# Performance work log

Measured on AMD Instinct MI355X. Metric: run time of the kernel, lower is better.

The kernel has to match this reference:

```python
import jax, jax.numpy as jnp
import numpy as np

L = 4          # num_layers
D = 512        # gconv_dim == tlayer_dim
HG, CG = 8, 64 # gconv heads, head dim (D//8)
HT, CT = 4, 128  # tlayer heads, head dim
FF = 4 * D
G, NPG = 128, 256
N = G * NPG
E = N * 16
AF, AV = 9, 64   # atom features / vocab
BF, BV = 3, 8    # bond features / vocab
OUT = 128
SCALE = 0.02


def setup_inputs() -> dict:
    key = jax.random.key(0)
    ks = iter(jax.random.split(key, 64))
    rn = lambda shape: (jax.random.normal(next(ks), shape, dtype=jnp.float32) * SCALE)
    inp = {}
    # float params (stacked over layers)
    inp['atom_emb'] = rn((AF, AV, D))
    inp['bond_emb'] = rn((BF, BV, D))
    for nm in ['gq_w', 'gk_w', 'gv_w', 'ge_w', 'gskip_w', 'mid_w']:
        inp[nm] = rn((L, D, D))
    for nm in ['gq_b', 'gk_b', 'gv_b', 'gskip_b', 'mid_b']:
        inp[nm] = rn((L, D))
    inp['mid_g'] = jnp.ones((L, D), jnp.float32)
    inp['mid_bt'] = jnp.zeros((L, D), jnp.float32)
    for nm in ['tq_w', 'tk_w', 'tv_w', 'to_w']:
        inp[nm] = rn((L, D, D))
    for nm in ['tq_b', 'tk_b', 'tv_b', 'to_b']:
        inp[nm] = rn((L, D))
    inp['ln1_g'] = jnp.ones((L, D), jnp.float32)
    inp['ln1_b'] = jnp.zeros((L, D), jnp.float32)
    inp['f1_w'] = rn((L, D, FF))
    inp['f1_b'] = rn((L, FF))
    inp['f2_w'] = rn((L, FF, D))
    inp['f2_b'] = rn((L, D))
    inp['ln2_g'] = jnp.ones((L, D), jnp.float32)
    inp['ln2_b'] = jnp.zeros((L, D), jnp.float32)
    inp['out_w'] = rn((D, OUT))
    inp['out_b'] = rn((OUT,))
    # int inputs
    inp['x'] = jax.random.randint(next(ks), (N, AF), 0, AV, dtype=jnp.int32)
    inp['edge_attr'] = jax.random.randint(next(ks), (E, BF), 0, BV, dtype=jnp.int32)
    # intra-graph edges: random offsets within each graph
    gid = jax.random.randint(next(ks), (E,), 0, G, dtype=jnp.int32)
    src = gid * NPG + jax.random.randint(next(ks), (E,), 0, NPG, dtype=jnp.int32)
    dst = gid * NPG + jax.random.randint(next(ks), (E,), 0, NPG, dtype=jnp.int32)
    inp['edge_index'] = jnp.stack([src, dst])
    inp['batch'] = jnp.repeat(jnp.arange(G, dtype=jnp.int32), NPG)
    return inp


def _ln(x, g, b, eps=1e-5):
    mu = x.mean(-1, keepdims=True)
    var = ((x - mu) ** 2).mean(-1, keepdims=True)
    return (x - mu) * jax.lax.rsqrt(var + eps) * g + b


def _forward(atom_emb, bond_emb, gq_w, gq_b, gk_w, gk_b, gv_w, gv_b, ge_w,
             gskip_w, gskip_b, mid_w, mid_b, mid_g, mid_bt,
             tq_w, tq_b, tk_w, tk_b, tv_w, tv_b, to_w, to_b,
             ln1_g, ln1_b, f1_w, f1_b, f2_w, f2_b, ln2_g, ln2_b,
             out_w, out_b, x, edge_index, edge_attr, batch):
    # encoders: sum of per-feature embeddings (OGB AtomEncoder/BondEncoder)
    h = atom_emb[jnp.arange(AF)[None, :], x].sum(1)          # [N, D]
    e_attr = bond_emb[jnp.arange(BF)[None, :], edge_attr].sum(1)  # [E, D]
    src, dst = edge_index[0], edge_index[1]

    for i in range(L):
        # --- TransformerConv (PyG): edge-conditioned multi-head graph attention
        q = (h @ gq_w[i] + gq_b[i]).reshape(N, HG, CG)
        k = (h @ gk_w[i] + gk_b[i]).reshape(N, HG, CG)
        v = (h @ gv_w[i] + gv_b[i]).reshape(N, HG, CG)
        ee = (e_attr @ ge_w[i]).reshape(E, HG, CG)           # lin_edge (no bias)
        ke = k[src] + ee
        ve = v[src] + ee
        logits = (q[dst] * ke).sum(-1) / np.sqrt(CG)          # [E, HG]
        m = jax.ops.segment_max(logits, dst, num_segments=N)
        p = jnp.exp(logits - m[dst])
        denom = jax.ops.segment_sum(p, dst, num_segments=N) + 1e-16
        alpha = p / denom[dst]
        agg = jax.ops.segment_sum(alpha[..., None] * ve, dst, num_segments=N)
        h = agg.reshape(N, D) + h @ gskip_w[i] + gskip_b[i]   # root skip
        # --- middle Linear + LayerNorm + ReLU
        h = jax.nn.relu(_ln(h @ mid_w[i] + mid_b[i], mid_g[i], mid_bt[i]))

    xg = h.reshape(G, NPG, D)
    for i in range(L):
        # --- transformer encoder layer, dense attention within each graph
        q = (xg @ tq_w[i] + tq_b[i]).reshape(G, NPG, HT, CT)
        k = (xg @ tk_w[i] + tk_b[i]).reshape(G, NPG, HT, CT)
        v = (xg @ tv_w[i] + tv_b[i]).reshape(G, NPG, HT, CT)
        attn = jax.nn.softmax(jnp.einsum('gqhc,gkhc->ghqk', q, k) / np.sqrt(CT), axis=-1)
        o = jnp.einsum('ghqk,gkhc->gqhc', attn, v).reshape(G, NPG, D)
        xg = _ln(xg + (o @ to_w[i] + to_b[i]), ln1_g[i], ln1_b[i])
        ff = jax.nn.relu(xg @ f1_w[i] + f1_b[i]) @ f2_w[i] + f2_b[i]
        xg = _ln(xg + ff, ln2_g[i], ln2_b[i])

    # mean readout over nodes per graph (segment mean via batch)
    hflat = xg.reshape(N, D)
    cnt = jax.ops.segment_sum(jnp.ones((N,), hflat.dtype), batch, num_segments=G)
    pooled = jax.ops.segment_sum(hflat, batch, num_segments=G) / cnt[:, None]
    return pooled @ out_w + out_b                              # [G, OUT]


def reference(atom_emb, bond_emb, gq_w, gq_b, gk_w, gk_b, gv_w, gv_b, ge_w,
              gskip_w, gskip_b, mid_w, mid_b, mid_g, mid_bt,
              tq_w, tq_b, tk_w, tk_b, tv_w, tv_b, to_w, to_b,
              ln1_g, ln1_b, f1_w, f1_b, f2_w, f2_b, ln2_g, ln2_b,
              out_w, out_b, x, edge_index, edge_attr, batch):
    return _forward(atom_emb, bond_emb, gq_w, gq_b, gk_w, gk_b, gv_w, gv_b, ge_w,
                    gskip_w, gskip_b, mid_w, mid_b, mid_g, mid_bt,
                    tq_w, tq_b, tk_w, tk_b, tv_w, tv_b, to_w, to_b,
                    ln1_g, ln1_b, f1_w, f1_b, f2_w, f2_b, ln2_g, ln2_b,
                    out_w, out_b, x, edge_index, edge_attr, batch)
```

## Files before the change

### kernel.cpp

```cpp
#include <hip/hip_runtime.h>
#include <hip/hip_bf16.h>
#include <math.h>

#define N_NODES 32768
#define DIM     512
#define NE      524288
#define NL      4
#define NG      128
#define NPG_    256
#define HG_     8
#define CG_     64
#define HT_     4
#define CT_     128
#define FF_     2048
#define AF_     9
#define AV_     64
#define BV_     8
#define OUTD    128

typedef unsigned short u16;
typedef __attribute__((ext_vector_type(8))) short bhalf8;
typedef __attribute__((ext_vector_type(4))) float floatx4;
typedef __attribute__((ext_vector_type(8))) unsigned short u16x8;
typedef __attribute__((ext_vector_type(4))) unsigned short u16x4;

__device__ __forceinline__ u16 f2bf(float f) {
  union { float f; unsigned u; } x; x.f = f;
  unsigned r = x.u + 0x7fffu + ((x.u >> 16) & 1u);
  return (u16)(r >> 16);
}
__device__ __forceinline__ float bf2f(u16 u) {
  union { unsigned u; float f; } x; x.u = ((unsigned)u) << 16; return x.f;
}

#define GL2LDS(gp, lp) __builtin_amdgcn_global_load_lds( \
    (const __attribute__((address_space(1))) unsigned int*)(gp), \
    (__attribute__((address_space(3))) unsigned int*)(lp), 16, 0, 0)

__global__ __launch_bounds__(128) void atom_enc_kernel(
    const float* __restrict__ emb, const int* __restrict__ x, u16* __restrict__ hb) {
  int n = blockIdx.x;
  int d4 = threadIdx.x;
  const int* xr = x + n * AF_;
  float4 acc = {0.f, 0.f, 0.f, 0.f};
#pragma unroll
  for (int f = 0; f < AF_; ++f) {
    int idx = xr[f];
    const float4 v = *(const float4*)&emb[((size_t)(f * AV_ + idx)) * DIM + 4 * d4];
    acc.x += v.x; acc.y += v.y; acc.z += v.z; acc.w += v.w;
  }
  u16x4 o;
  o[0] = f2bf(acc.x); o[1] = f2bf(acc.y); o[2] = f2bf(acc.z); o[3] = f2bf(acc.w);
  *(u16x4*)&hb[(size_t)n * DIM + 4 * d4] = o;
}

__global__ __launch_bounds__(512) void bemb_proj_kernel(
    const float* __restrict__ bond_emb, const float* __restrict__ gew, u16* __restrict__ tab) {
  __shared__ float red[8][64];
  int r = blockIdx.x;
  int col = (threadIdx.x & 63) + blockIdx.y * 64;
  int kp = threadIdx.x >> 6;
  const float* a = bond_emb + (size_t)r * DIM + kp * 64;
  const float* w = gew + (size_t)kp * 64 * DIM + col;
  float acc = 0.f;
#pragma unroll 8
  for (int kx = 0; kx < 64; ++kx)
    acc += a[kx] * w[(size_t)kx * DIM];
  red[kp][threadIdx.x & 63] = acc;
  __syncthreads();
  if (threadIdx.x < 64) {
    float s = 0.f;
#pragma unroll
    for (int p = 0; p < 8; ++p) s += red[p][threadIdx.x];
    tab[(size_t)r * DIM + col] = f2bf(s);
  }
}

__global__ __launch_bounds__(256) void wcvt_kernel(
    const float* __restrict__ W, u16* __restrict__ Wt, int K, int N) {
  __shared__ float t[32][33];
  const size_t mo = (size_t)blockIdx.z * K * N;
  int k0 = blockIdx.y * 32, n0 = blockIdx.x * 32;
  int tx = threadIdx.x & 31, ty = threadIdx.x >> 5;
#pragma unroll
  for (int i = 0; i < 32; i += 8)
    t[ty + i][tx] = W[mo + (size_t)(k0 + ty + i) * N + n0 + tx];
  __syncthreads();
#pragma unroll
  for (int i = 0; i < 32; i += 8)
    Wt[mo + (size_t)(n0 + ty + i) * K + k0 + tx] = f2bf(t[tx][ty + i]);
}

__global__ __launch_bounds__(256) void gemm_mfma_kernel(
    const u16* __restrict__ A, const u16* __restrict__ Bt,
    const float* __restrict__ bias, float* __restrict__ Cf, u16* __restrict__ Cb,
    int K, int Nout, int relu, int bf16out, int vtout) {
  __shared__ __align__(16) u16 As[4096];
  __shared__ __align__(16) u16 Bs[4096];
  const int tid = threadIdx.x;
  const int wave = tid >> 6, lane = tid & 63;
  const int bm = blockIdx.y * 128, bn = blockIdx.x * 128;
  const int wr = wave >> 1, wc = wave & 1;

  const size_t rowA = (size_t)bm + (tid >> 2);
  const size_t rowB = (size_t)bn + (tid >> 2);
  const int gofs = (tid & 3) * 8;
  const u16* pA = A + rowA * K + gofs;
  const u16* pB = Bt + rowB * K + gofs;
  u16* lA0 = &As[wave * 512];
  u16* lB0 = &Bs[wave * 512];
  const size_t skip64 = (size_t)64 * K;

  floatx4 acc[4][4] = {};
  const int r = lane & 15, kg = lane >> 4;
  const int aoff = (wr * 64 + r) * 32 + kg * 8;
  const int boff = (wc * 64 + r) * 32 + kg * 8;

  for (int k0 = 0; k0 < K; k0 += 32) {
    GL2LDS(pA + k0, lA0);
    GL2LDS(pA + skip64 + k0, lA0 + 2048);
    GL2LDS(pB + k0, lB0);
    GL2LDS(pB + skip64 + k0, lB0 + 2048);
    __syncthreads();
    bhalf8 af[4], bg[4];
#pragma unroll
    for (int mi = 0; mi < 4; ++mi) af[mi] = *(const bhalf8*)&As[aoff + mi * 512];
#pragma unroll
    for (int ni = 0; ni < 4; ++ni) bg[ni] = *(const bhalf8*)&Bs[boff + ni * 512];
#pragma unroll
    for (int mi = 0; mi < 4; ++mi)
#pragma unroll
      for (int ni = 0; ni < 4; ++ni)
        acc[mi][ni] = __builtin_amdgcn_mfma_f32_16x16x32_bf16(af[mi], bg[ni], acc[mi][ni], 0, 0, 0);
    __syncthreads();
  }

  const int rb = (lane >> 4) * 4;
  const int cc = lane & 15;
#pragma unroll
  for (int mi = 0; mi < 4; ++mi) {
#pragma unroll
    for (int ni = 0; ni < 4; ++ni) {
      int gr0 = bm + wr * 64 + mi * 16 + rb;
      int gc = bn + wc * 64 + ni * 16 + cc;
      float bv = bias[gc];
#pragma unroll
      for (int reg = 0; reg < 4; ++reg) {
        int gr = gr0 + reg;
        float v = acc[mi][ni][reg] + bv;
        if (relu) v = fmaxf(v, 0.f);
        if (vtout)        Cb[((size_t)(gr >> 8) * DIM + gc) * NPG_ + (gr & 255)] = f2bf(v);
        else if (bf16out) Cb[(size_t)gr * Nout + gc] = f2bf(v);
        else              Cf[(size_t)gr * Nout + gc] = v;
      }
    }
  }
}

__global__ __launch_bounds__(256) void attn_s_mfma_kernel(
    const u16* __restrict__ q, const u16* __restrict__ k, u16* __restrict__ S, int zbase) {
  __shared__ __align__(16) u16 As[4096];
  __shared__ __align__(16) u16 Bs[4096];
  const int tid = threadIdx.x;
  const int wave = tid >> 6, lane = tid & 63;
  const int zl = blockIdx.z, z = zbase + zl, g = z >> 2, hh = z & 3;
  const int bm = blockIdx.y * 128, bn = blockIdx.x * 128;
  const int wr = wave >> 1, wc = wave & 1;
  const u16* qg = q + (size_t)g * NPG_ * DIM + hh * CT_;
  const u16* kg2 = k + (size_t)g * NPG_ * DIM + hh * CT_;
  const u16* pA = qg + (size_t)(bm + (tid >> 2)) * DIM + (tid & 3) * 8;
  const u16* pB = kg2 + (size_t)(bn + (tid >> 2)) * DIM + (tid & 3) * 8;
  u16* lA0 = &As[wave * 512];
  u16* lB0 = &Bs[wave * 512];
  const size_t skip64 = (size_t)64 * DIM;
  floatx4 acc[4][4] = {};
  const int r = lane & 15, kg_ = lane >> 4;
  const int aoff = (wr * 64 + r) * 32 + kg_ * 8;
  const int boff = (wc * 64 + r) * 32 + kg_ * 8;
  for (int k0 = 0; k0 < CT_; k0 += 32) {
    GL2LDS(pA + k0, lA0);
    GL2LDS(pA + skip64 + k0, lA0 + 2048);
    GL2LDS(pB + k0, lB0);
    GL2LDS(pB + skip64 + k0, lB0 + 2048);
    __syncthreads();
    bhalf8 af[4], bg[4];
#pragma unroll
    for (int mi = 0; mi < 4; ++mi) af[mi] = *(const bhalf8*)&As[aoff + mi * 512];
#pragma unroll
    for (int ni = 0; ni < 4; ++ni) bg[ni] = *(const bhalf8*)&Bs[boff + ni * 512];
#pragma unroll
    for (int mi = 0; mi < 4; ++mi)
#pragma unroll
      for (int ni = 0; ni < 4; ++ni)
        acc[mi][ni] = __builtin_amdgcn_mfma_f32_16x16x32_bf16(af[mi], bg[ni], acc[mi][ni], 0, 0, 0);
    __syncthreads();
  }
  const float sc = 0.08838834764831845f;
  u16* C = S + (size_t)zl * NPG_ * NPG_;
  const int rb = (lane >> 4) * 4, cc = lane & 15;
#pragma unroll
  for (int mi = 0; mi < 4; ++mi)
#pragma unroll
    for (int ni = 0; ni < 4; ++ni) {
      int gr = bm + wr * 64 + mi * 16 + rb;
      int gc = bn + wc * 64 + ni * 16 + cc;
#pragma unroll
      for (int reg = 0; reg < 4; ++reg)
        C[(size_t)(gr + reg) * NPG_ + gc] = f2bf(acc[mi][ni][reg] * sc);
    }
}

__global__ __launch_bounds__(256) void softmax256_kernel(u16* __restrict__ SP) {
  size_t row = (size_t)blockIdx.x * 4 + (threadIdx.x >> 6);
  int lane = threadIdx.x & 63;
  u16* r = SP + row * NPG_;
  u16x4 v = *(u16x4*)&r[lane * 4];
  float x0 = bf2f(v[0]), x1 = bf2f(v[1]), x2 = bf2f(v[2]), x3 = bf2f(v[3]);
  float m = fmaxf(fmaxf(x0, x1), fmaxf(x2, x3));
#pragma unroll
  for (int off = 32; off; off >>= 1) m = fmaxf(m, __shfl_xor(m, off));
  x0 = expf(x0 - m); x1 = expf(x1 - m); x2 = expf(x2 - m); x3 = expf(x3 - m);
  float s = x0 + x1 + x2 + x3;
#pragma unroll
  for (int off = 32; off; off >>= 1) s += __shfl_xor(s, off);
  float inv = 1.0f / s;
  u16x4 o;
  o[0] = f2bf(x0 * inv); o[1] = f2bf(x1 * inv);
  o[2] = f2bf(x2 * inv); o[3] = f2bf(x3 * inv);
  *(u16x4*)&r[lane * 4] = o;
}

__global__ __launch_bounds__(256) void attn_o_mfma_kernel(
    const u16* __restrict__ P, const u16* __restrict__ vt, u16* __restrict__ O, int zbase) {
  __shared__ __align__(16) u16 As[4096];
  __shared__ __align__(16) u16 Bs[4096];
  const int tid = threadIdx.x;
  const int wave = tid >> 6, lane = tid & 63;
  const int zl = blockIdx.z, z = zbase + zl, g = z >> 2, hh = z & 3;
  const int bm = blockIdx.y * 128;
  const int wr = wave >> 1, wc = wave & 1;
  const u16* A = P + (size_t)zl * NPG_ * NPG_;
  const u16* Bt = vt + ((size_t)g * DIM + hh * CT_) * NPG_;
  const u16* pA = A + (size_t)(bm + (tid >> 2)) * NPG_ + (tid & 3) * 8;
  const u16* pB = Bt + (size_t)(tid >> 2) * NPG_ + (tid & 3) * 8;
  u16* lA0 = &As[wave * 512];
  u16* lB0 = &Bs[wave * 512];
  const size_t skip64 = (size_t)64 * NPG_;
  floatx4 acc[4][4] = {};
  const int r = lane & 15, kg_ = lane >> 4;
  const int aoff = (wr * 64 + r) * 32 + kg_ * 8;
  const int boff = (wc * 64 + r) * 32 + kg_ * 8;
  for (int k0 = 0; k0 < NPG_; k0 += 32) {
    GL2LDS(pA + k0, lA0);
    GL2LDS(pA + skip64 + k0, lA0 + 2048);
    GL2LDS(pB + k0, lB0);
    GL2LDS(pB + skip64 + k0, lB0 + 2048);
    __syncthreads();
    bhalf8 af[4], bg[4];
#pragma unroll
    for (int mi = 0; mi < 4; ++mi) af[mi] = *(const bhalf8*)&As[aoff + mi * 512];
#pragma unroll
    for (int ni = 0; ni < 4; ++ni) bg[ni] = *(const bhalf8*)&Bs[boff + ni * 512];
#pragma unroll
    for (int mi = 0; mi < 4; ++mi)
#pragma unroll
      for (int ni = 0; ni < 4; ++ni)
        acc[mi][ni] = __builtin_amdgcn_mfma_f32_16x16x32_bf16(af[mi], bg[ni], acc[mi][ni], 0, 0, 0);
    __syncthreads();
  }
  u16* C = O + ((size_t)g * NPG_) * DIM + hh * CT_;
  const int rb = (lane >> 4) * 4, cc = lane & 15;
#pragma unroll
  for (int mi = 0; mi < 4; ++mi)
#pragma unroll
    for (int ni = 0; ni < 4; ++ni) {
      int gr = bm + wr * 64 + mi * 16 + rb;
      int gc = wc * 64 + ni * 16 + cc;
#pragma unroll
      for (int reg = 0; reg < 4; ++reg)
        C[(size_t)(gr + reg) * DIM + gc] = f2bf(acc[mi][ni][reg]);
    }
}

__global__ __launch_bounds__(256) void gemm_bias_kernel(
    const float* __restrict__ A, const float* __restrict__ W,
    const float* __restrict__ bias, float* __restrict__ C,
    int M, int K, int Nout, int relu) {
  __shared__ float As[16][65];
  __shared__ float Bs[16][64];
  const int bm = blockIdx.y * 64;
  const int bn = blockIdx.x * 64;
  const int tid = threadIdx.x;
  const int tx = tid & 15, ty = tid >> 4;
  float acc[4][4] = {};
  for (int k0 = 0; k0 < K; k0 += 16) {
    {
      int row = tid >> 2;
      int kq = (tid & 3) << 2;
      float4 a = *(const float4*)&A[(size_t)(bm + row) * K + k0 + kq];
      As[kq + 0][row] = a.x; As[kq + 1][row] = a.y; As[kq + 2][row] = a.z; As[kq + 3][row] = a.w;
    }
    {
      int krow = tid >> 4;
      int cq = (tid & 15) << 2;
      *(float4*)&Bs[krow][cq] = *(const float4*)&W[(size_t)(k0 + krow) * Nout + bn + cq];
    }
    __syncthreads();
#pragma unroll
    for (int kk = 0; kk < 16; ++kk) {
      float a[4];
#pragma unroll
      for (int i = 0; i < 4; ++i) a[i] = As[kk][ty * 4 + i];
      float4 b4 = *(const float4*)&Bs[kk][tx * 4];
      float b[4] = {b4.x, b4.y, b4.z, b4.w};
#pragma unroll
      for (int i = 0; i < 4; ++i)
#pragma unroll
        for (int j = 0; j < 4; ++j) acc[i][j] = fmaf(a[i], b[j], acc[i][j]);
    }
    __syncthreads();
  }
  float4 bv = *(const float4*)&bias[bn + tx * 4];
#pragma unroll
  for (int i = 0; i < 4; ++i) {
    int row = bm + ty * 4 + i;
    float4 o;
    o.x = acc[i][0] + bv.x; o.y = acc[i][1] + bv.y;
    o.z = acc[i][2] + bv.z; o.w = acc[i][3] + bv.w;
    if (relu) {
      o.x = fmaxf(o.x, 0.f); o.y = fmaxf(o.y, 0.f);
      o.z = fmaxf(o.z, 0.f); o.w = fmaxf(o.w, 0.f);
    }
    *(float4*)&C[(size_t)row * Nout + bn + tx * 4] = o;
  }
}

__global__ __launch_bounds__(256) void deg_count_kernel(const int* __restrict__ ei, int* __restrict__ deg) {
  int e = blockIdx.x * 256 + threadIdx.x;
  atomicAdd(&deg[ei[NE + e]], 1);
}

__global__ __launch_bounds__(1024) void scan_kernel(const int* __restrict__ deg, int* __restrict__ rp) {
  __shared__ int sums[1024];
  int t = threadIdx.x;
  int base = t * 32;
  int local[32];
  int s = 0;
#pragma unroll
  for (int i = 0; i < 32; ++i) { local[i] = s; s += deg[base + i]; }
  sums[t] = s;
  __syncthreads();
  for (int off = 1; off < 1024; off <<= 1) {
    int other = (t >= off) ? sums[t - off] : 0;
    __syncthreads();
    sums[t] += other;
    __syncthreads();
  }
  int chunk_off = sums[t] - s;
#pragma unroll
  for (int i = 0; i < 32; ++i) rp[base + i] = chunk_off + local[i];
  if (t == 1023) rp[N_NODES] = sums[1023];
}

__global__ __launch_bounds__(256) void scatter_kernel(
    const int* __restrict__ ei, const int* __restrict__ rp,
    int* __restrict__ cur, int* __restrict__ csr) {
  int e = blockIdx.x * 256 + threadIdx.x;
  int d = ei[NE + e];
  int pos = atomicAdd(&cur[d], 1);
  csr[rp[d] + pos] = e;
}

__global__ __launch_bounds__(256) void edge_logits_kernel(
    const u16* __restrict__ q, const u16* __restrict__ k, const u16* __restrict__ tab,
    const int* __restrict__ ei, const int* __restrict__ ea, float* __restrict__ logits) {
  int e = blockIdx.x * 4 + (threadIdx.x >> 6);
  int lane = threadIdx.x & 63;
  int src = ei[e], dst = ei[NE + e];
  int a0 = ea[e * 3], a1 = ea[e * 3 + 1], a2 = ea[e * 3 + 2];
  const u16x8 qv = *(const u16x8*)&q[(size_t)dst * DIM + lane * 8];
  const u16x8 kv = *(const u16x8*)&k[(size_t)src * DIM + lane * 8];
  const size_t to = (size_t)lane * 8;
  const u16x8 e0 = *(const u16x8*)&tab[(size_t)a0 * DIM + to];
  const u16x8 e1 = *(const u16x8*)&tab[(size_t)(8 + a1) * DIM + to];
  const u16x8 e2 = *(const u16x8*)&tab[(size_t)(16 + a2) * DIM + to];
  float acc = 0.f;
#pragma unroll
  for (int j = 0; j < 8; ++j) {
    float ee = bf2f(e0[j]) + bf2f(e1[j]) + bf2f(e2[j]);
    acc += bf2f(qv[j]) * (bf2f(kv[j]) + ee);
  }
  acc += __shfl_xor(acc, 1);
  acc += __shfl_xor(acc, 2);
  acc += __shfl_xor(acc, 4);
  if ((lane & 7) == 0) logits[(size_t)e * HG_ + (lane >> 3)] = acc * 0.125f;
}

#define CHUNK 128
__global__ __launch_bounds__(512) void edge_agg_kernel(
    const u16* __restrict__ v, const u16* __restrict__ tab, const float* __restrict__ logits,
    const float* __restrict__ skip, const int* __restrict__ ei, const int* __restrict__ ea,
    const int* __restrict__ rp, const int* __restrict__ csr, u16* __restrict__ hnew) {
  int n = blockIdx.x;
  int d = threadIdx.x;
  int hh = d >> 6;
  int lane = d & 63;
  int start = rp[n];
  int deg = rp[n + 1] - start;
  __shared__ int s_eid[CHUNK];
  __shared__ int s_src[CHUNK];
  __shared__ int s_ea[CHUNK];
  __shared__ float s_p[CHUNK * HG_];
  __shared__ float s_w[24 * HG_];
  __shared__ float s_max[HG_];
  __shared__ float s_resc[HG_];
  if (d < 24 * HG_) s_w[d] = 0.f;
  if (d < HG_) s_max[d] = -3.0e38f;
  float accum = 0.f, den = 0.f;
  for (int c0 = 0; c0 < deg; c0 += CHUNK) {
    int cnt = min(CHUNK, deg - c0);
    __syncthreads();
    if (d < cnt) {
      int eid = csr[start + c0 + d];
      s_eid[d] = eid;
      s_src[d] = ei[eid];
      s_ea[d] = ea[eid * 3] | (ea[eid * 3 + 1] << 8) | (ea[eid * 3 + 2] << 16);
    }
    __syncthreads();
    for (int jh = d; jh < cnt * HG_; jh += 512)
      s_p[jh] = logits[(size_t)s_eid[jh >> 3] * HG_ + (jh & 7)];
    __syncthreads();
    float cm = -3.0e38f;
    for (int j = lane; j < cnt; j += 64)
      cm = fmaxf(cm, s_p[j * HG_ + hh]);
#pragma unroll
    for (int off = 32; off; off >>= 1) cm = fmaxf(cm, __shfl_xor(cm, off));
    if (lane == 0) {
      float om = s_max[hh];
      float nm = fmaxf(om, cm);
      s_resc[hh] = (nm > om) ? expf(om - nm) : 1.0f;
      s_max[hh] = nm;
    }
    __syncthreads();
    float rsc = s_resc[hh];
    accum *= rsc;
    den *= rsc;
    if (d < 24 * HG_) s_w[d] *= s_resc[d & 7];
    __syncthreads();
    for (int jh = d; jh < cnt * HG_; jh += 512) {
      int h2 = jh & 7;
      float p = expf(s_p[jh] - s_max[h2]);
      s_p[jh] = p;
      int eap = s_ea[jh >> 3];
      atomicAdd(&s_w[(eap & 0xff) * HG_ + h2], p);
      atomicAdd(&s_w[(8 + ((eap >> 8) & 0xff)) * HG_ + h2], p);
      atomicAdd(&s_w[(16 + (eap >> 16)) * HG_ + h2], p);
    }
    __syncthreads();
    for (int j = 0; j < cnt; ++j) {
      float p = s_p[j * HG_ + hh];
      den += p;
      accum = fmaf(p, bf2f(v[(size_t)s_src[j] * DIM + d]), accum);
    }
  }
  __syncthreads();
#pragma unroll
  for (int r2 = 0; r2 < 24; ++r2)
    accum = fmaf(s_w[r2 * HG_ + hh], bf2f(tab[(size_t)r2 * DIM + d]), accum);
  size_t o = (size_t)n * DIM + d;
  hnew[o] = f2bf(accum / (den + 1e-16f) + skip[o]);
}

__global__ __launch_bounds__(256) void ln_kernel(
    const float* __restrict__ in, const u16* __restrict__ resid,
    const float* __restrict__ g, const float* __restrict__ b,
    u16* __restrict__ outb, int relu) {
  int row = blockIdx.x * 4 + (threadIdx.x >> 6);
  int lane = threadIdx.x & 63;
  size_t base = (size_t)row * DIM + lane * 8;
  float x[8];
  {
    float4 v0 = *(const float4*)&in[base];
    float4 v1 = *(const float4*)&in[base + 4];
    x[0] = v0.x; x[1] = v0.y; x[2] = v0.z; x[3] = v0.w;
    x[4] = v1.x; x[5] = v1.y; x[6] = v1.z; x[7] = v1.w;
  }
  if (resid) {
    u16x8 rv = *(const u16x8*)&resid[base];
#pragma unroll
    for (int i = 0; i < 8; ++i) x[i] += bf2f(rv[i]);
  }
  float s = 0.f;
#pragma unroll
  for (int i = 0; i < 8; ++i) s += x[i];
#pragma unroll
  for (int off = 32; off; off >>= 1) s += __shfl_xor(s, off);
  float mu = s * (1.0f / DIM);
  float vs = 0.f;
#pragma unroll
  for (int i = 0; i < 8; ++i) { float t = x[i] - mu; vs += t * t; }
#pragma unroll
  for (int off = 32; off; off >>= 1) vs += __shfl_xor(vs, off);
  float rstd = 1.0f / sqrtf(vs * (1.0f / DIM) + 1e-5f);
  float4 g0 = *(const float4*)&g[lane * 8];
  float4 g1 = *(const float4*)&g[lane * 8 + 4];
  float4 b0 = *(const float4*)&b[lane * 8];
  float4 b1 = *(const float4*)&b[lane * 8 + 4];
  float gg[8] = {g0.x, g0.y, g0.z, g0.w, g1.x, g1.y, g1.z, g1.w};
  float bb[8] = {b0.x, b0.y, b0.z, b0.w, b1.x, b1.y, b1.z, b1.w};
  u16x8 ob;
#pragma unroll
  for (int i = 0; i < 8; ++i) {
    float y = (x[i] - mu) * rstd * gg[i] + bb[i];
    if (relu) y = fmaxf(y, 0.f);
    ob[i] = f2bf(y);
  }
  *(u16x8*)&outb[base] = ob;
}

__global__ __launch_bounds__(512) void pool_kernel(const u16* __restrict__ xg, float* __restrict__ pooled) {
  int g = blockIdx.x;
  int d = threadIdx.x;
  float acc = 0.f;
  for (int p = 0; p < NPG_; ++p) acc += bf2f(xg[((size_t)g * NPG_ + p) * DIM + d]);
  pooled[(size_t)g * DIM + d] = acc * (1.0f / NPG_);
}

extern "C" void kernel_launch(void* const* d_in, const int* in_sizes, int n_in,
                              void* d_out, int out_size, void* d_ws, size_t ws_size,
                              hipStream_t stream) {
  const float* atom_emb = (const float*)d_in[0];
  const float* bond_emb = (const float*)d_in[1];
  const float* gq_w = (const float*)d_in[2];
  const float* gk_w = (const float*)d_in[3];
  const float* gv_w = (const float*)d_in[4];
  const float* ge_w = (const float*)d_in[5];
  const float* gskip_w = (const float*)d_in[6];
  const float* mid_w = (const float*)d_in[7];
  const float* gq_b = (const float*)d_in[8];
  const float* gk_b = (const float*)d_in[9];
  const float* gv_b = (const float*)d_in[10];
  const float* gskip_b = (const float*)d_in[11];
  const float* mid_b = (const float*)d_in[12];
  const float* mid_g = (const float*)d_in[13];
  const float* mid_bt = (const float*)d_in[14];
  const float* tq_w = (const float*)d_in[15];
  const float* tk_w = (const float*)d_in[16];
  const float* tv_w = (const float*)d_in[17];
  const float* to_w = (const float*)d_in[18];
  const float* tq_b = (const float*)d_in[19];
  const float* tk_b = (const float*)d_in[20];
  const float* tv_b = (const float*)d_in[21];
  const float* to_b = (const float*)d_in[22];
  const float* ln1_g = (const float*)d_in[23];
  const float* ln1_b = (const float*)d_in[24];
  const float* f1_w = (const float*)d_in[25];
  const float* f1_b = (const float*)d_in[26];
  const float* f2_w = (const float*)d_in[27];
  const float* f2_b = (const float*)d_in[28];
  const float* ln2_g = (const float*)d_in[29];
  const float* ln2_b = (const float*)d_in[30];
  const float* out_w = (const float*)d_in[31];
  const float* out_b = (const float*)d_in[32];
  const int* x = (const int*)d_in[33];
  const int* ea = (const int*)d_in[34];
  const int* ei = (const int*)d_in[35];

  char* wbase = (char*)d_ws;
  size_t woff = 0;
  auto ALLOC = [&](size_t bytes) -> void* {
    void* r = wbase + woff;
    woff += (bytes + 255) & ~(size_t)255;
    return r;
  };
  const size_t ND = (size_t)N_NODES * DIM * sizeof(float);
  const size_t NDH = (size_t)N_NODES * DIM * sizeof(u16);
  u16*   wt     = (u16*)ALLOC((size_t)17825792 * sizeof(u16));
  u16*   hb     = (u16*)ALLOC(NDH);
  u16*   Abuf   = (u16*)ALLOC(NDH);
  u16*   Bbuf   = (u16*)ALLOC(NDH);
  u16*   Cbuf   = (u16*)ALLOC(NDH);
  float* E      = (float*)ALLOC(ND);
  u16*   U      = (u16*)ALLOC((size_t)16777216);
  u16*   tab    = (u16*)ALLOC(24 * DIM * sizeof(u16));
  float* pooled = (float*)ALLOC((size_t)NG * DIM * sizeof(float));
  int* deg      = (int*)ALLOC(N_NODES * sizeof(int));
  int* cur      = (int*)ALLOC(N_NODES * sizeof(int));
  int* rp       = (int*)ALLOC((N_NODES + 1) * sizeof(int));
  int* csr      = (int*)ALLOC((size_t)NE * sizeof(int));
  (void)ws_size; (void)in_sizes; (void)n_in; (void)out_size;

  const size_t DD = (size_t)DIM * DIM;
  const size_t DD4 = 4 * DD;
  u16* gqT = wt;            u16* gkT = wt + DD4;      u16* gvT = wt + 2 * DD4;
  u16* gskipT = wt + 3*DD4; u16* midT = wt + 4 * DD4;
  u16* tqT = wt + 5 * DD4;  u16* tkT = wt + 6 * DD4;  u16* tvT = wt + 7 * DD4;
  u16* toT = wt + 8 * DD4;
  u16* f1T = wt + 9 * DD4;
  u16* f2T = f1T + (size_t)4 * DIM * FF_;

  auto wcvt = [&](const float* W, u16* Wt, int K, int N, int L2) {
    dim3 grid(N / 32, K / 32, L2);
    wcvt_kernel<<<grid, 256, 0, stream>>>(W, Wt, K, N);
  };
  auto mgemm = [&](const u16* A_, const u16* Bt_, const float* bias_,
                   float* Cf_, u16* Cb_, int M_, int K_, int Nout_,
                   int relu_, int bf16o_, int vtout_) {
    dim3 grid(Nout_ / 128, M_ / 128);
    gemm_mfma_kernel<<<grid, 256, 0, stream>>>(A_, Bt_, bias_, Cf_, Cb_, K_, Nout_, relu_, bf16o_, vtout_);
  };

  wcvt(gq_w, gqT, DIM, DIM, 4);   wcvt(gk_w, gkT, DIM, DIM, 4);
  wcvt(gv_w, gvT, DIM, DIM, 4);   wcvt(gskip_w, gskipT, DIM, DIM, 4);
  wcvt(mid_w, midT, DIM, DIM, 4);
  wcvt(tq_w, tqT, DIM, DIM, 4);   wcvt(tk_w, tkT, DIM, DIM, 4);
  wcvt(tv_w, tvT, DIM, DIM, 4);   wcvt(to_w, toT, DIM, DIM, 4);
  wcvt(f1_w, f1T, DIM, FF_, 4);   wcvt(f2_w, f2T, FF_, DIM, 4);

  hipMemsetAsync(deg, 0, N_NODES * sizeof(int), stream);
  hipMemsetAsync(cur, 0, N_NODES * sizeof(int), stream);
  deg_count_kernel<<<NE / 256, 256, 0, stream>>>(ei, deg);
  scan_kernel<<<1, 1024, 0, stream>>>(deg, rp);
  scatter_kernel<<<NE / 256, 256, 0, stream>>>(ei, rp, cur, csr);

  atom_enc_kernel<<<N_NODES, 128, 0, stream>>>(atom_emb, x, hb);

  for (int i = 0; i < NL; ++i) {
    bemb_proj_kernel<<<dim3(24, 8), 512, 0, stream>>>(bond_emb, ge_w + i * DD, tab);
    mgemm(hb, gqT + i * DD, gq_b + i * DIM, nullptr, Abuf, N_NODES, DIM, DIM, 0, 1, 0);
    mgemm(hb, gkT + i * DD, gk_b + i * DIM, nullptr, Bbuf, N_NODES, DIM, DIM, 0, 1, 0);
    mgemm(hb, gvT + i * DD, gv_b + i * DIM, nullptr, Cbuf, N_NODES, DIM, DIM, 0, 1, 0);
    mgemm(hb, gskipT + i * DD, gskip_b + i * DIM, E, nullptr, N_NODES, DIM, DIM, 0, 0, 0);
    edge_logits_kernel<<<NE / 4, 256, 0, stream>>>(Abuf, Bbuf, tab, ei, ea, (float*)U);
    edge_agg_kernel<<<N_NODES, 512, 0, stream>>>(Cbuf, tab, (float*)U, E, ei, ea, rp, csr, Abuf);
    mgemm(Abuf, midT + i * DD, mid_b + i * DIM, E, nullptr, N_NODES, DIM, DIM, 0, 0, 0);
    ln_kernel<<<N_NODES / 4, 256, 0, stream>>>(E, nullptr, mid_g + i * DIM, mid_bt + i * DIM, hb, 1);
  }

  for (int i = 0; i < NL; ++i) {
    mgemm(hb, tqT + i * DD, tq_b + i * DIM, nullptr, Abuf, N_NODES, DIM, DIM, 0, 1, 0);
    mgemm(hb, tkT + i * DD, tk_b + i * DIM, nullptr, Bbuf, N_NODES, DIM, DIM, 0, 1, 0);
    mgemm(hb, tvT + i * DD, tv_b + i * DIM, nullptr, Cbuf, N_NODES, DIM, DIM, 0, 1, 1);
    for (int rnd = 0; rnd < 4; ++rnd) {
      attn_s_mfma_kernel<<<dim3(2, 2, 128), 256, 0, stream>>>(Abuf, Bbuf, U, rnd * 128);
      softmax256_kernel<<<(128 * NPG_) / 4, 256, 0, stream>>>(U);
      attn_o_mfma_kernel<<<dim3(1, 2, 128), 256, 0, stream>>>(U, Cbuf, Abuf, rnd * 128);
    }
    mgemm(Abuf, toT + i * DD, to_b + i * DIM, E, nullptr, N_NODES, DIM, DIM, 0, 0, 0);
    ln_kernel<<<N_NODES / 4, 256, 0, stream>>>(E, hb, ln1_g + i * DIM, ln1_b + i * DIM, hb, 0);
    for (int c = 0; c < 4; ++c) {
      mgemm(hb + (size_t)c * 8192 * DIM, f1T + (size_t)i * DIM * FF_, f1_b + i * FF_,
            nullptr, Abuf, 8192, DIM, FF_, 1, 1, 0);
      mgemm(Abuf, f2T + (size_t)i * FF_ * DIM, f2_b + i * DIM,
            E + (size_t)c * 8192 * DIM, nullptr, 8192, FF_, DIM, 0, 0, 0);
    }
    ln_kernel<<<N_NODES / 4, 256, 0, stream>>>(E, hb, ln2_g + i * DIM, ln2_b + i * DIM, hb, 0);
  }

  pool_kernel<<<NG, 512, 0, stream>>>(hb, pooled);
  gemm_bias_kernel<<<dim3(OUTD / 64, NG / 64), 256, 0, stream>>>(pooled, out_w, out_b, (float*)d_out, NG, DIM, OUTD, 0);
}
```

Baseline: 5.624 ms.

## Fuse Q/K/V/skip projections into one GEMM and edge logits into aggregation

Weights for the gconv q/k/v/skip projections and the transformer q/k/v projections are laid out contiguously so each set runs as one wide GEMM. The epilogue routes each 512-column segment to its own output buffer and bias. The separate edge_logits kernel is removed, and its logits are now computed inside edge_agg, with q cached in shared memory per destination node. This cuts kernel launches, re-reads of the input activations, and the round-trip of the logits buffer through global memory, at the cost of a more branchy GEMM epilogue and more per-edge gather work inside the aggregation kernel.

```diff
diff --git a/kernel.cpp b/kernel.cpp
--- a/kernel.cpp
+++ b/kernel.cpp
@@ -77,14 +77,15 @@
 }
 
 __global__ __launch_bounds__(256) void wcvt_kernel(
-    const float* __restrict__ W, u16* __restrict__ Wt, int K, int N) {
+    const float* __restrict__ W, u16* __restrict__ Wt, int K, int N, size_t ostride) {
   __shared__ float t[32][33];
-  const size_t mo = (size_t)blockIdx.z * K * N;
+  const size_t mi = (size_t)blockIdx.z * K * N;
+  const size_t mo = (size_t)blockIdx.z * ostride;
   int k0 = blockIdx.y * 32, n0 = blockIdx.x * 32;
   int tx = threadIdx.x & 31, ty = threadIdx.x >> 5;
 #pragma unroll
   for (int i = 0; i < 32; i += 8)
-    t[ty + i][tx] = W[mo + (size_t)(k0 + ty + i) * N + n0 + tx];
+    t[ty + i][tx] = W[mi + (size_t)(k0 + ty + i) * N + n0 + tx];
   __syncthreads();
 #pragma unroll
   for (int i = 0; i < 32; i += 8)
@@ -93,8 +94,11 @@
 
 __global__ __launch_bounds__(256) void gemm_mfma_kernel(
     const u16* __restrict__ A, const u16* __restrict__ Bt,
-    const float* __restrict__ bias, float* __restrict__ Cf, u16* __restrict__ Cb,
-    int K, int Nout, int relu, int bf16out, int vtout) {
+    const float* __restrict__ bias, const float* __restrict__ bias1,
+    const float* __restrict__ bias2, const float* __restrict__ bias3,
+    float* __restrict__ Cf, u16* __restrict__ Cb,
+    u16* __restrict__ R1, u16* __restrict__ R2, float* __restrict__ R3f,
+    int K, int Nout, int relu, int bf16out, int vtout, int route) {
   __shared__ __align__(16) u16 As[4096];
   __shared__ __align__(16) u16 Bs[4096];
   const int tid = threadIdx.x;
@@ -137,21 +141,43 @@
 
   const int rb = (lane >> 4) * 4;
   const int cc = lane & 15;
+  const int seg = (route != 0) ? (bn >> 9) : 0;
+  const float* bp = bias;
+  if (route != 0) {
+    if (seg == 1) bp = bias1;
+    else if (seg == 2) bp = bias2;
+    else if (seg == 3) bp = bias3;
+  }
 #pragma unroll
   for (int mi = 0; mi < 4; ++mi) {
 #pragma unroll
     for (int ni = 0; ni < 4; ++ni) {
       int gr0 = bm + wr * 64 + mi * 16 + rb;
       int gc = bn + wc * 64 + ni * 16 + cc;
-      float bv = bias[gc];
+      int c = (route != 0) ? (gc & 511) : gc;
+      float bv = bp[c];
 #pragma unroll
       for (int reg = 0; reg < 4; ++reg) {
         int gr = gr0 + reg;
         float v = acc[mi][ni][reg] + bv;
         if (relu) v = fmaxf(v, 0.f);
-        if (vtout)        Cb[((size_t)(gr >> 8) * DIM + gc) * NPG_ + (gr & 255)] = f2bf(v);
-        else if (bf16out) Cb[(size_t)gr * Nout + gc] = f2bf(v);
-        else              Cf[(size_t)gr * Nout + gc] = v;
+        if (route == 1) {
+          size_t idx = (size_t)gr * 512 + c;
+          if (seg == 0)      Cb[idx] = f2bf(v);
+          else if (seg == 1) R1[idx] = f2bf(v);
+          else if (seg == 2) R2[idx] = f2bf(v);
+          else               R3f[idx] = v;
+        } else if (route == 2) {
+          if (seg == 0)      Cb[(size_t)gr * 512 + c] = f2bf(v);
+          else if (seg == 1) R1[(size_t)gr * 512 + c] = f2bf(v);
+          else               R2[((size_t)(gr >> 8) * DIM + c) * NPG_ + (gr & 255)] = f2bf(v);
+        } else if (vtout) {
+          Cb[((size_t)(gr >> 8) * DIM + gc) * NPG_ + (gr & 255)] = f2bf(v);
+        } else if (bf16out) {
+          Cb[(size_t)gr * Nout + gc] = f2bf(v);
+        } else {
+          Cf[(size_t)gr * Nout + gc] = v;
+        }
       }
     }
   }
@@ -371,35 +397,11 @@
   csr[rp[d] + pos] = e;
 }
 
-__global__ __launch_bounds__(256) void edge_logits_kernel(
-    const u16* __restrict__ q, const u16* __restrict__ k, const u16* __restrict__ tab,
-    const int* __restrict__ ei, const int* __restrict__ ea, float* __restrict__ logits) {
-  int e = blockIdx.x * 4 + (threadIdx.x >> 6);
-  int lane = threadIdx.x & 63;
-  int src = ei[e], dst = ei[NE + e];
-  int a0 = ea[e * 3], a1 = ea[e * 3 + 1], a2 = ea[e * 3 + 2];
-  const u16x8 qv = *(const u16x8*)&q[(size_t)dst * DIM + lane * 8];
-  const u16x8 kv = *(const u16x8*)&k[(size_t)src * DIM + lane * 8];
-  const size_t to = (size_t)lane * 8;
-  const u16x8 e0 = *(const u16x8*)&tab[(size_t)a0 * DIM + to];
-  const u16x8 e1 = *(const u16x8*)&tab[(size_t)(8 + a1) * DIM + to];
-  const u16x8 e2 = *(const u16x8*)&tab[(size_t)(16 + a2) * DIM + to];
-  float acc = 0.f;
-#pragma unroll
-  for (int j = 0; j < 8; ++j) {
-    float ee = bf2f(e0[j]) + bf2f(e1[j]) + bf2f(e2[j]);
-    acc += bf2f(qv[j]) * (bf2f(kv[j]) + ee);
-  }
-  acc += __shfl_xor(acc, 1);
-  acc += __shfl_xor(acc, 2);
-  acc += __shfl_xor(acc, 4);
-  if ((lane & 7) == 0) logits[(size_t)e * HG_ + (lane >> 3)] = acc * 0.125f;
-}
-
 #define CHUNK 128
 __global__ __launch_bounds__(512) void edge_agg_kernel(
-    const u16* __restrict__ v, const u16* __restrict__ tab, const float* __restrict__ logits,
-    const float* __restrict__ skip, const int* __restrict__ ei, const int* __restrict__ ea,
+    const u16* __restrict__ q, const u16* __restrict__ k, const u16* __restrict__ v,
+    const u16* __restrict__ tab, const float* __restrict__ skip,
+    const int* __restrict__ ei, const int* __restrict__ ea,
     const int* __restrict__ rp, const int* __restrict__ csr, u16* __restrict__ hnew) {
   int n = blockIdx.x;
   int d = threadIdx.x;
@@ -407,13 +409,14 @@
   int lane = d & 63;
   int start = rp[n];
   int deg = rp[n + 1] - start;
-  __shared__ int s_eid[CHUNK];
   __shared__ int s_src[CHUNK];
   __shared__ int s_ea[CHUNK];
   __shared__ float s_p[CHUNK * HG_];
+  __shared__ float s_q[DIM];
   __shared__ float s_w[24 * HG_];
   __shared__ float s_max[HG_];
   __shared__ float s_resc[HG_];
+  s_q[d] = bf2f(q[(size_t)n * DIM + d]);
   if (d < 24 * HG_) s_w[d] = 0.f;
   if (d < HG_) s_max[d] = -3.0e38f;
   float accum = 0.f, den = 0.f;
@@ -422,13 +425,29 @@
     __syncthreads();
     if (d < cnt) {
       int eid = csr[start + c0 + d];
-      s_eid[d] = eid;
       s_src[d] = ei[eid];
       s_ea[d] = ea[eid * 3] | (ea[eid * 3 + 1] << 8) | (ea[eid * 3 + 2] << 16);
     }
     __syncthreads();
-    for (int jh = d; jh < cnt * HG_; jh += 512)
-      s_p[jh] = logits[(size_t)s_eid[jh >> 3] * HG_ + (jh & 7)];
+    for (int j = hh; j < cnt; j += 8) {
+      int srcn = s_src[j];
+      int eap = s_ea[j];
+      const u16x8 kv = *(const u16x8*)&k[(size_t)srcn * DIM + lane * 8];
+      const size_t to = (size_t)lane * 8;
+      const u16x8 e0 = *(const u16x8*)&tab[(size_t)(eap & 0xff) * DIM + to];
+      const u16x8 e1 = *(const u16x8*)&tab[(size_t)(8 + ((eap >> 8) & 0xff)) * DIM + to];
+      const u16x8 e2 = *(const u16x8*)&tab[(size_t)(16 + (eap >> 16)) * DIM + to];
+      float acc = 0.f;
+#pragma unroll
+      for (int jj = 0; jj < 8; ++jj) {
+        float ee = bf2f(e0[jj]) + bf2f(e1[jj]) + bf2f(e2[jj]);
+        acc += s_q[lane * 8 + jj] * (bf2f(kv[jj]) + ee);
+      }
+      acc += __shfl_xor(acc, 1);
+      acc += __shfl_xor(acc, 2);
+      acc += __shfl_xor(acc, 4);
+      if ((lane & 7) == 0) s_p[j * HG_ + (lane >> 3)] = acc * 0.125f;
+    }
     __syncthreads();
     float cm = -3.0e38f;
     for (int j = lane; j < cnt; j += 64)
@@ -591,31 +610,37 @@
   (void)ws_size; (void)in_sizes; (void)n_in; (void)out_size;
 
   const size_t DD = (size_t)DIM * DIM;
-  const size_t DD4 = 4 * DD;
-  u16* gqT = wt;            u16* gkT = wt + DD4;      u16* gvT = wt + 2 * DD4;
-  u16* gskipT = wt + 3*DD4; u16* midT = wt + 4 * DD4;
-  u16* tqT = wt + 5 * DD4;  u16* tkT = wt + 6 * DD4;  u16* tvT = wt + 7 * DD4;
-  u16* toT = wt + 8 * DD4;
-  u16* f1T = wt + 9 * DD4;
-  u16* f2T = f1T + (size_t)4 * DIM * FF_;
-
-  auto wcvt = [&](const float* W, u16* Wt, int K, int N, int L2) {
+  u16* gfT  = wt;
+  u16* midT = wt + 16 * DD;
+  u16* tfT  = wt + 20 * DD;
+  u16* toT  = wt + 32 * DD;
+  u16* f1T  = wt + 36 * DD;
+  u16* f2T  = wt + 52 * DD;
+
+  auto wcvt = [&](const float* W, u16* Wt, int K, int N, int L2, size_t ostride) {
     dim3 grid(N / 32, K / 32, L2);
-    wcvt_kernel<<<grid, 256, 0, stream>>>(W, Wt, K, N);
+    wcvt_kernel<<<grid, 256, 0, stream>>>(W, Wt, K, N, ostride);
   };
   auto mgemm = [&](const u16* A_, const u16* Bt_, const float* bias_,
                    float* Cf_, u16* Cb_, int M_, int K_, int Nout_,
                    int relu_, int bf16o_, int vtout_) {
     dim3 grid(Nout_ / 128, M_ / 128);
-    gemm_mfma_kernel<<<grid, 256, 0, stream>>>(A_, Bt_, bias_, Cf_, Cb_, K_, Nout_, relu_, bf16o_, vtout_);
+    gemm_mfma_kernel<<<grid, 256, 0, stream>>>(A_, Bt_, bias_, nullptr, nullptr, nullptr,
+                                               Cf_, Cb_, nullptr, nullptr, nullptr,
+                                               K_, Nout_, relu_, bf16o_, vtout_, 0);
   };
 
-  wcvt(gq_w, gqT, DIM, DIM, 4);   wcvt(gk_w, gkT, DIM, DIM, 4);
-  wcvt(gv_w, gvT, DIM, DIM, 4);   wcvt(gskip_w, gskipT, DIM, DIM, 4);
-  wcvt(mid_w, midT, DIM, DIM, 4);
-  wcvt(tq_w, tqT, DIM, DIM, 4);   wcvt(tk_w, tkT, DIM, DIM, 4);
-  wcvt(tv_w, tvT, DIM, DIM, 4);   wcvt(to_w, toT, DIM, DIM, 4);
-  wcvt(f1_w, f1T, DIM, FF_, 4);   wcvt(f2_w, f2T, FF_, DIM, 4);
+  wcvt(gq_w, gfT + 0 * DD, DIM, DIM, 4, 4 * DD);
+  wcvt(gk_w, gfT + 1 * DD, DIM, DIM, 4, 4 * DD);
+  wcvt(gv_w, gfT + 2 * DD, DIM, DIM, 4, 4 * DD);
+  wcvt(gskip_w, gfT + 3 * DD, DIM, DIM, 4, 4 * DD);
+  wcvt(mid_w, midT, DIM, DIM, 4, DD);
+  wcvt(tq_w, tfT + 0 * DD, DIM, DIM, 4, 3 * DD);
+  wcvt(tk_w, tfT + 1 * DD, DIM, DIM, 4, 3 * DD);
+  wcvt(tv_w, tfT + 2 * DD, DIM, DIM, 4, 3 * DD);
+  wcvt(to_w, toT, DIM, DIM, 4, DD);
+  wcvt(f1_w, f1T, DIM, FF_, 4, 4 * DD);
+  wcvt(f2_w, f2T, FF_, DIM, 4, 4 * DD);
 
   hipMemsetAsync(deg, 0, N_NODES * sizeof(int), stream);
   hipMemsetAsync(cur, 0, N_NODES * sizeof(int), stream);
@@ -627,20 +652,28 @@
 
   for (int i = 0; i < NL; ++i) {
     bemb_proj_kernel<<<dim3(24, 8), 512, 0, stream>>>(bond_emb, ge_w + i * DD, tab);
-    mgemm(hb, gqT + i * DD, gq_b + i * DIM, nullptr, Abuf, N_NODES, DIM, DIM, 0, 1, 0);
-    mgemm(hb, gkT + i * DD, gk_b + i * DIM, nullptr, Bbuf, N_NODES, DIM, DIM, 0, 1, 0);
-    mgemm(hb, gvT + i * DD, gv_b + i * DIM, nullptr, Cbuf, N_NODES, DIM, DIM, 0, 1, 0);
-    mgemm(hb, gskipT + i * DD, gskip_b + i * DIM, E, nullptr, N_NODES, DIM, DIM, 0, 0, 0);
-    edge_logits_kernel<<<NE / 4, 256, 0, stream>>>(Abuf, Bbuf, tab, ei, ea, (float*)U);
-    edge_agg_kernel<<<N_NODES, 512, 0, stream>>>(Cbuf, tab, (float*)U, E, ei, ea, rp, csr, Abuf);
+    {
+      dim3 grid(2048 / 128, N_NODES / 128);
+      gemm_mfma_kernel<<<grid, 256, 0, stream>>>(
+          hb, gfT + (size_t)i * 4 * DD,
+          gq_b + i * DIM, gk_b + i * DIM, gv_b + i * DIM, gskip_b + i * DIM,
+          nullptr, Abuf, Bbuf, Cbuf, E,
+          DIM, 2048, 0, 0, 0, 1);
+    }
+    edge_agg_kernel<<<N_NODES, 512, 0, stream>>>(Abuf, Bbuf, Cbuf, tab, E, ei, ea, rp, csr, Abuf);
     mgemm(Abuf, midT + i * DD, mid_b + i * DIM, E, nullptr, N_NODES, DIM, DIM, 0, 0, 0);
     ln_kernel<<<N_NODES / 4, 256, 0, stream>>>(E, nullptr, mid_g + i * DIM, mid_bt + i * DIM, hb, 1);
   }
 
   for (int i = 0; i < NL; ++i) {
-    mgemm(hb, tqT + i * DD, tq_b + i * DIM, nullptr, Abuf, N_NODES, DIM, DIM, 0, 1, 0);
-    mgemm(hb, tkT + i * DD, tk_b + i * DIM, nullptr, Bbuf, N_NODES, DIM, DIM, 0, 1, 0);
-    mgemm(hb, tvT + i * DD, tv_b + i * DIM, nullptr, Cbuf, N_NODES, DIM, DIM, 0, 1, 1);
+    {
+      dim3 grid(1536 / 128, N_NODES / 128);
+      gemm_mfma_kernel<<<grid, 256, 0, stream>>>(
+          hb, tfT + (size_t)i * 3 * DD,
+          tq_b + i * DIM, tk_b + i * DIM, tv_b + i * DIM, nullptr,
+          nullptr, Abuf, Bbuf, Cbuf, nullptr,
+          DIM, 1536, 0, 0, 0, 2);
+    }
     for (int rnd = 0; rnd < 4; ++rnd) {
       attn_s_mfma_kernel<<<dim3(2, 2, 128), 256, 0, stream>>>(Abuf, Bbuf, U, rnd * 128);
       softmax256_kernel<<<(128 * NPG_) / 4, 256, 0, stream>>>(U);
@@ -649,9 +682,9 @@
     mgemm(Abuf, toT + i * DD, to_b + i * DIM, E, nullptr, N_NODES, DIM, DIM, 0, 0, 0);
     ln_kernel<<<N_NODES / 4, 256, 0, stream>>>(E, hb, ln1_g + i * DIM, ln1_b + i * DIM, hb, 0);
     for (int c = 0; c < 4; ++c) {
-      mgemm(hb + (size_t)c * 8192 * DIM, f1T + (size_t)i * DIM * FF_, f1_b + i * FF_,
+      mgemm(hb + (size_t)c * 8192 * DIM, f1T + (size_t)i * 4 * DD, f1_b + i * FF_,
             nullptr, Abuf, 8192, DIM, FF_, 1, 1, 0);
-      mgemm(Abuf, f2T + (size_t)i * FF_ * DIM, f2_b + i * DIM,
+      mgemm(Abuf, f2T + (size_t)i * 4 * DD, f2_b + i * DIM,
             E + (size_t)c * 8192 * DIM, nullptr, 8192, FF_, DIM, 0, 0, 0);
     }
     ln_kernel<<<N_NODES / 4, 256, 0, stream>>>(E, hb, ln2_g + i * DIM, ln2_b + i * DIM, hb, 0);
```

Measured after the change: 6.107 ms. 8.6% more time.
